# Kernel tuning notes

Measured on AMD Instinct MI355X. Metric: run time of the kernel, lower is better.

## Reference

```python
import math
import jax, jax.numpy as jnp
import numpy as np

B, N, D_MODEL, H = 2, 4096, 2048, 16
HEAD_DIM = D_MODEL // H
CHUNK = 128  # chunk length for the lightning-attention recurrence


def _slopes(n_heads):
    # ALiBi-style slopes used by lightning attention (n_heads is a power of 2)
    start = 2.0 ** (-(2.0 ** -(math.log2(n_heads) - 3)))
    return np.array([start ** (i + 1) for i in range(n_heads)], dtype=np.float32)


def setup_inputs() -> dict:
    key = jax.random.key(0)
    kx, k1, k2, k3, k4 = jax.random.split(key, 5)
    scale = 1.0 / math.sqrt(D_MODEL)
    x = jax.random.normal(kx, (B, N, D_MODEL), dtype=jnp.float32)
    w_qkv = jax.random.normal(k1, (3 * D_MODEL, D_MODEL), dtype=jnp.float32) * scale
    b_qkv = jax.random.normal(k2, (3 * D_MODEL,), dtype=jnp.float32) * 0.01
    w_out = jax.random.normal(k3, (D_MODEL, D_MODEL), dtype=jnp.float32) * scale
    b_out = jax.random.normal(k4, (D_MODEL,), dtype=jnp.float32) * 0.01
    return {"x": x, "w_qkv": w_qkv, "b_qkv": b_qkv, "w_out": w_out, "b_out": b_out}


def _lightning_attn(q, k, v):
    # q,k,v: (B, H, N, d). Causal linear attention with per-head decay lam:
    #   S_t = lam * S_{t-1} + k_t v_t^T ;  o_t = q_t S_t
    b, h, n, d = q.shape
    nc = n // CHUNK
    lam = jnp.exp(-jnp.asarray(_slopes(h)))  # (H,)

    pos = jnp.arange(CHUNK, dtype=jnp.float32)
    decay_q = lam[:, None] ** (pos + 1.0)            # (H, C) inter-chunk q scaling
    decay_k = lam[:, None] ** (CHUNK - 1.0 - pos)    # (H, C) state-update k scaling
    diff = pos[:, None] - pos[None, :]
    causal = diff >= 0
    dmask = jnp.where(causal, lam[:, None, None] ** jnp.maximum(diff, 0.0), 0.0)  # (H,C,C)
    lam_c = lam ** CHUNK                              # (H,)

    def to_chunks(t):
        return t.reshape(b, h, nc, CHUNK, d).transpose(2, 0, 1, 3, 4)  # (nc,B,H,C,d)

    qc, kc, vc = to_chunks(q), to_chunks(k), to_chunks(v)

    def step(S, inp):
        qb, kb, vb = inp  # each (B,H,C,d); S: (B,H,d,d)
        inter = jnp.einsum('bhcd,bhde->bhce', qb * decay_q[None, :, :, None], S)
        scores = jnp.einsum('bhcd,bhed->bhce', qb, kb) * dmask[None]
        intra = jnp.einsum('bhce,bhed->bhcd', scores, vb)
        S_new = lam_c[None, :, None, None] * S + jnp.einsum(
            'bhcd,bhce->bhde', kb * decay_k[None, :, :, None], vb)
        return S_new, inter + intra

    S0 = jnp.zeros((b, h, d, d), dtype=q.dtype)
    _, out = jax.lax.scan(step, S0, (qc, kc, vc))  # out: (nc,B,H,C,d)
    return out.transpose(1, 2, 0, 3, 4).reshape(b, h, n, d)


def reference(x, w_qkv, b_qkv, w_out, b_out):
    b, n, dm = x.shape
    qkv = x @ w_qkv.T + b_qkv                         # (B,N,3D)
    q, k, v = jnp.split(qkv, 3, axis=-1)
    def heads(t):
        return t.reshape(b, n, H, HEAD_DIM).transpose(0, 2, 1, 3)  # (B,H,N,d)
    attn = _lightning_attn(heads(q), heads(k), heads(v))
    attn = attn.transpose(0, 2, 1, 3).reshape(b, n, dm)
    return attn @ w_out.T + b_out
```

## Files before the change

kernel.cpp:

```cpp
#include <hip/hip_runtime.h>
#include <stdint.h>

#define DM    2048
#define NSEQ  4096
#define BB    2
#define NH    16
#define HD    128
#define CHK   128
#define NCHK  32
#define NBH   (BB*NH)
#define MTOT  (BB*NSEQ)
#define N3    (3*DM)

typedef unsigned short u16;
typedef unsigned int   u32;
typedef __attribute__((ext_vector_type(8))) short s16x8;
typedef __attribute__((ext_vector_type(4))) short s16x4;
typedef __attribute__((ext_vector_type(4))) float f32x4;
typedef __attribute__((ext_vector_type(2))) unsigned short u16x2;

__device__ __forceinline__ float b2f(u16 b){ u32 u = ((u32)b) << 16; float f; __builtin_memcpy(&f,&u,4); return f; }
__device__ __forceinline__ u16 f2b(float f){ u32 u; __builtin_memcpy(&u,&f,4); u += 0x7fffu + ((u>>16)&1u); return (u16)(u>>16); }

__device__ __forceinline__ void gload16(const u16* g, u16* l){
  __builtin_amdgcn_global_load_lds((const __attribute__((address_space(1))) void*)g,
                                   (__attribute__((address_space(3))) void*)l, 16, 0, 0);
}

__global__ __launch_bounds__(256) void conv_bf16(const float* __restrict__ src,
                                                 u16* __restrict__ dst, int n4)
{
  for (int i = blockIdx.x*blockDim.x + threadIdx.x; i < n4; i += gridDim.x*blockDim.x){
    f32x4 v = *(const f32x4*)(src + (size_t)i*4);
    s16x4 o;
    #pragma unroll
    for (int j=0;j<4;j++) o[j] = (short)f2b(v[j]);
    *(s16x4*)(dst + (size_t)i*4) = o;
  }
}


#define GEMM256_CORE(GA_, GB_)                                                  \
  const int tid  = threadIdx.x;                                                 \
  const int lane = tid & 63;                                                    \
  const int w    = tid >> 6;                                                    \
  const int wm_i = w >> 2, wn_i = w & 3;                                        \
  const int m0 = blockIdx.y << 8;                                               \
  const int n0 = blockIdx.x << 8;                                               \
                  \
  const int q_  = (lane*16) ^ (((lane>>5)&1) << 5);                             \
  const int sgr = q_ >> 6;                                                      \
  const int sgc = (q_ & 63) >> 1;                                               \
  const u16* gA = GA_ + (size_t)(m0 + w*32 + sgr)*DM + sgc;                     \
  const u16* gB = GB_ + (size_t)(n0 + w*32 + sgr)*DM + sgc;                     \
  const int l15 = lane & 15, lg = lane >> 4;                                    \
  const int swz = ((lg*16) ^ (((l15>>3)&1) << 5)) >> 1;          \
  const int arow = (wm_i*128 + l15)*32 + swz;                                   \
  const int brow = (wn_i*64  + l15)*32 + swz;                                   \
  f32x4 acc[8][4];                                                              \
  _Pragma("unroll")                                                             \
  for (int m=0;m<8;m++)                                                         \
    _Pragma("unroll")                                                           \
    for (int n=0;n<4;n++) acc[m][n] = f32x4{0.f,0.f,0.f,0.f};                   \
  s16x8 bfr[4];                                                                 \
  auto STAGE_A = [&](int set, int kt){                                          \
    const u16* a = gA + kt*32;                                                  \
    u16* la = lds + set + w*1024;                                               \
    gload16(a,         la);                                                     \
    gload16(a + 16*DM, la + 512);                                               \
  };                                                                            \
  auto STAGE_B = [&](int set, int kt){                                          \
    const u16* b = gB + kt*32;                                                  \
    u16* la = lds + set + w*1024;                                               \
    gload16(b,         la + 8192);                                              \
    gload16(b + 16*DM, la + 8704);                                              \
  };                                                                            \
  auto COMPA = [&](int set){                                                    \
    const u16* base = lds + set;                                                \
    s16x8 af[4];                                                                \
    _Pragma("unroll")                                                           \
    for (int n=0;n<4;n++) bfr[n] = *(const s16x8*)(base + 8192 + brow + n*512); \
    _Pragma("unroll")                                                           \
    for (int m=0;m<4;m++) af[m] = *(const s16x8*)(base + arow + m*512);         \
    __builtin_amdgcn_s_setprio(1);                                              \
    _Pragma("unroll")                                                           \
    for (int m=0;m<4;m++)                                                       \
      _Pragma("unroll")                                                         \
      for (int n=0;n<4;n++)                                                     \
        acc[m][n] = __builtin_amdgcn_mfma_f32_16x16x32_bf16(af[m], bfr[n], acc[m][n], 0,0,0); \
    __builtin_amdgcn_s_setprio(0);                                              \
  };                                                                            \
  auto COMPB = [&](int set){                                                    \
    const u16* base = lds + set;                                                \
    s16x8 af[4];                                                                \
    _Pragma("unroll")                                                           \
    for (int m=0;m<4;m++) af[m] = *(const s16x8*)(base + arow + (m+4)*512);     \
    __builtin_amdgcn_s_setprio(1);                                              \
    _Pragma("unroll")                                                           \
    for (int m=0;m<4;m++)                                                       \
      _Pragma("unroll")                                                         \
      for (int n=0;n<4;n++)                                                     \
        acc[m+4][n] = __builtin_amdgcn_mfma_f32_16x16x32_bf16(af[m], bfr[n], acc[m+4][n], 0,0,0); \
    __builtin_amdgcn_s_setprio(0);                                              \
  };                                                                            \
  STAGE_A(0, 0);     STAGE_B(0, 0);                                             \
  STAGE_A(16384, 1); STAGE_B(16384, 1);                                         \
  STAGE_A(32768, 2); STAGE_B(32768, 2);                                         \
  asm volatile("s_waitcnt vmcnt(8)" ::: "memory");                              \
  __builtin_amdgcn_s_barrier();                                                 \
  int s0=0, s1=16384, s2=32768, s3=49152;                                       \
  for (int t=0; t<64; ++t){                                                     \
    if (t < 61) STAGE_A(s3, t+3);                                               \
    COMPA(s0);                                                                  \
    __builtin_amdgcn_s_barrier();                                               \
    if (t < 61) STAGE_B(s3, t+3);                                               \
    COMPB(s0);                                                                  \
    if      (t < 61)  { asm volatile("s_waitcnt vmcnt(8)" ::: "memory"); }      \
    else if (t == 61) { asm volatile("s_waitcnt vmcnt(4)" ::: "memory"); }      \
    else if (t == 62) { asm volatile("s_waitcnt vmcnt(0)" ::: "memory"); }      \
    __builtin_amdgcn_s_barrier();                                               \
    const int tmp=s0; s0=s1; s1=s2; s2=s3; s3=tmp;                              \
  }

__global__ __launch_bounds__(512, 2) void gemm_qkv(const u16* __restrict__ Xb,
    const u16* __restrict__ Wb, const float* __restrict__ bias,
    u16* __restrict__ Qb, u16* __restrict__ Kb, u16* __restrict__ Vb)
{
  __shared__ u16 lds[4*16384];
  GEMM256_CORE(Xb, Wb)

  #pragma unroll
  for (int n=0;n<4;n++){
    const int gn = n0 + wn_i*64 + n*16 + l15;
    const float bv = bias[gn];
    const int which = gn >> 11;
    const int h = (gn >> 7) & 15;
    const int e = gn & 127;
    u16* base_ = (which==0) ? Qb : ((which==1) ? Kb : Vb);
    #pragma unroll
    for (int m=0;m<8;m++){
      #pragma unroll
      for (int r=0;r<4;r++){
        const int gm = m0 + wm_i*128 + m*16 + lg*4 + r;
        const int b  = gm >> 12;
        const int tt = gm & (NSEQ-1);
        base_[(((size_t)(b*NH + h))*NSEQ + tt)*HD + e] = f2b(acc[m][n][r] + bv);
      }
    }
  }
}

__global__ __launch_bounds__(512, 2) void gemm_out(const u16* __restrict__ Ab,
    const u16* __restrict__ Wb, const float* __restrict__ bias,
    float* __restrict__ Out)
{
  __shared__ u16 lds[4*16384];
  GEMM256_CORE(Ab, Wb)

  #pragma unroll
  for (int n=0;n<4;n++){
    const int gn = n0 + wn_i*64 + n*16 + l15;
    const float bv = bias[gn];
    #pragma unroll
    for (int m=0;m<8;m++){
      #pragma unroll
      for (int r=0;r<4;r++){
        const int gm = m0 + wm_i*128 + m*16 + lg*4 + r;
        Out[(size_t)gm*DM + gn] = acc[m][n][r] + bv;
      }
    }
  }
}

__global__ __launch_bounds__(256) void chunk_kv(const u16* __restrict__ Kb,
    const u16* __restrict__ Vb, u16* __restrict__ USb)
{
  __shared__ short Kt[128][152];
  __shared__ short Vt[128][152];
  const int tid = threadIdx.x;
  const int blk = blockIdx.x;
  const int c  = blk & (NCHK-1);
  const int bh = blk >> 5;
  const int h  = bh & (NH-1);
  const float slope = exp2f(-0.5f*(float)(h+1));

  const u16* kg = Kb + ((size_t)bh*NSEQ + (size_t)c*CHK)*HD;
  const u16* vg = Vb + ((size_t)bh*NSEQ + (size_t)c*CHK)*HD;

  const int e0 = (tid & 63) * 2;
  const int tq = tid >> 6;
  #pragma unroll
  for (int it=0; it<4; it++){
    const int tb = it*32 + tq*8;
    s16x8 k0v, k1v, v0v, v1v;
    #pragma unroll
    for (int j=0;j<8;j++){
      const int t = tb + j;
      u16x2 kv = *(const u16x2*)(kg + (size_t)t*HD + e0);
      u16x2 vv = *(const u16x2*)(vg + (size_t)t*HD + e0);
      const float dk = expf(-slope*(float)(CHK-1-t));
      k0v[j] = (short)f2b(b2f(kv[0])*dk);
      k1v[j] = (short)f2b(b2f(kv[1])*dk);
      v0v[j] = (short)vv[0];
      v1v[j] = (short)vv[1];
    }
    *(s16x8*)&Kt[e0  ][tb] = k0v;
    *(s16x8*)&Kt[e0+1][tb] = k1v;
    *(s16x8*)&Vt[e0  ][tb] = v0v;
    *(s16x8*)&Vt[e0+1][tb] = v1v;
  }
  __syncthreads();

  const int lane = tid & 63;
  const int l15 = lane & 15, lg = lane >> 4;
  const int w = tid >> 6;
  const int wm = (w >> 1) << 6, wn = (w & 1) << 6;
  f32x4 acc[4][4];
  #pragma unroll
  for (int i=0;i<4;i++)
    #pragma unroll
    for (int j=0;j<4;j++) acc[i][j] = f32x4{0.f,0.f,0.f,0.f};

  #pragma unroll
  for (int ks=0; ks<4; ks++){
    const int kk = ks*32 + lg*8;
    s16x8 af[4], bf[4];
    #pragma unroll
    for (int m=0;m<4;m++) af[m] = *(const s16x8*)&Kt[wm + m*16 + l15][kk];
    #pragma unroll
    for (int n=0;n<4;n++) bf[n] = *(const s16x8*)&Vt[wn + n*16 + l15][kk];
    #pragma unroll
    for (int m=0;m<4;m++)
      #pragma unroll
      for (int n=0;n<4;n++)
        acc[m][n] = __builtin_amdgcn_mfma_f32_16x16x32_bf16(af[m], bf[n], acc[m][n], 0,0,0);
  }

  u16* up = USb + (size_t)blk*(HD*HD);
  #pragma unroll
  for (int m=0;m<4;m++)
    #pragma unroll
    for (int n=0;n<4;n++)
      #pragma unroll
      for (int r=0;r<4;r++){
        const int d = wm + m*16 + lg*4 + r;
        const int f = wn + n*16 + l15;
        up[d*HD + f] = f2b(acc[m][n][r]);
      }
}

__global__ __launch_bounds__(256) void scan_state(u16* __restrict__ USb)
{
  const int bh = blockIdx.x >> 3;
  const int rs = blockIdx.x & 7;
  const int tid = threadIdx.x;
  const int h = bh & (NH-1);
  const float slope = exp2f(-0.5f*(float)(h+1));
  const float lamC = expf(-slope*(float)CHK);
  float s[8];
  #pragma unroll
  for (int i=0;i<8;i++) s[i]=0.f;
  u16* base = USb + (size_t)bh*NCHK*HD*HD + rs*2048;
  const int off = tid*8;
  for (int c=0;c<NCHK;c++){
    u16* p = base + (size_t)c*HD*HD + off;
    s16x8 u = *(const s16x8*)p;
    s16x8 wv;
    #pragma unroll
    for (int j=0;j<8;j++) wv[j] = (short)f2b(s[j]);
    *(s16x8*)p = wv;
    #pragma unroll
    for (int j=0;j<8;j++) s[j] = lamC*s[j] + b2f((u16)u[j]);
  }
}

__global__ __launch_bounds__(512) void attn_chunk(
    const u16* __restrict__ Qb, const u16* __restrict__ Kb, const u16* __restrict__ Vb,
    const u16* __restrict__ Sb, u16* __restrict__ ATT)
{
  __shared__ short lds[73728];
  short* Qs = lds;
  short* Ks = lds + 17408;
  short* Vt = lds + 34816;
  short* St = lds + 54272;

  const int tid = threadIdx.x;
  const int blk = blockIdx.x;
  const int c  = blk & (NCHK-1);
  const int bh = blk >> 5;
  const int b  = bh >> 4, h = bh & 15;
  const float slope = exp2f(-0.5f*(float)(h+1));

  const size_t qoff = ((size_t)bh*NSEQ + (size_t)c*CHK)*HD;

  #pragma unroll
  for (int i=0;i<4;i++){
    const int lin = i*4096 + tid*8;
    const int r = lin >> 7, e = lin & 127;
    *(s16x8*)&Qs[r*136 + e] = *(const s16x8*)(Qb + qoff + lin);
    *(s16x8*)&Ks[r*136 + e] = *(const s16x8*)(Kb + qoff + lin);
  }
  {
    const int f0 = (tid & 63)*2;
    const int tq = tid >> 6;
    const u16* vg = Vb + qoff;
    const u16* sg = Sb + ((size_t)bh*NCHK + c)*HD*HD;
    #pragma unroll
    for (int it=0; it<2; it++){
      const int t0 = it*64 + tq*8;
      s16x8 v0v, v1v, s0v, s1v;
      #pragma unroll
      for (int j=0;j<8;j++){
        u16x2 v2 = *(const u16x2*)(vg + (size_t)(t0+j)*HD + f0);
        u16x2 s2 = *(const u16x2*)(sg + (size_t)(t0+j)*HD + f0);
        v0v[j]=(short)v2[0]; v1v[j]=(short)v2[1];
        s0v[j]=(short)s2[0]; s1v[j]=(short)s2[1];
      }
      *(s16x8*)&Vt[(f0  )*152 + t0] = v0v;
      *(s16x8*)&Vt[(f0+1)*152 + t0] = v1v;
      *(s16x8*)&St[(f0  )*152 + t0] = s0v;
      *(s16x8*)&St[(f0+1)*152 + t0] = s1v;
    }
  }
  __syncthreads();

  const int lane = tid & 63;
  const int l15 = lane & 15, lg = lane >> 4;
  const int w = tid >> 6;
  const int wrow = (w >> 1) << 5;
  const int wcol = (w & 1) << 6;

  f32x4 accs[2][4], acco[2][4];
  #pragma unroll
  for (int m=0;m<2;m++)
    #pragma unroll
    for (int n=0;n<4;n++){ accs[m][n]=f32x4{0.f,0.f,0.f,0.f}; acco[m][n]=f32x4{0.f,0.f,0.f,0.f}; }

  #pragma unroll
  for (int ks=0; ks<4; ks++){
    const int kk = ks*32 + lg*8;
    s16x8 qa[2], kb_[4], sb_[4];
    #pragma unroll
    for (int m=0;m<2;m++) qa[m] = *(const s16x8*)&Qs[(wrow + m*16 + l15)*136 + kk];
    #pragma unroll
    for (int n=0;n<4;n++){
      kb_[n] = *(const s16x8*)&Ks[(wcol + n*16 + l15)*136 + kk];
      sb_[n] = *(const s16x8*)&St[(wcol + n*16 + l15)*152 + kk];
    }
    #pragma unroll
    for (int m=0;m<2;m++)
      #pragma unroll
      for (int n=0;n<4;n++){
        accs[m][n] = __builtin_amdgcn_mfma_f32_16x16x32_bf16(qa[m], kb_[n], accs[m][n], 0,0,0);
        acco[m][n] = __builtin_amdgcn_mfma_f32_16x16x32_bf16(qa[m], sb_[n], acco[m][n], 0,0,0);
      }
  }
  __syncthreads();

  #pragma unroll
  for (int m=0;m<2;m++){
    #pragma unroll
    for (int r=0;r<4;r++){
      const int t = wrow + m*16 + lg*4 + r;
      const float dq = expf(-slope*(float)(t+1));
      #pragma unroll
      for (int n=0;n<4;n++){
        const int s = wcol + n*16 + l15;
        float v = accs[m][n][r];
        v = (t >= s) ? v*expf(-slope*(float)(t-s)) : 0.f;
        Ks[t*136 + s] = (short)f2b(v);
        acco[m][n][r] *= dq;
      }
    }
  }
  __syncthreads();

  #pragma unroll
  for (int ks=0; ks<4; ks++){
    const int kk = ks*32 + lg*8;
    s16x8 sa[2], vb_[4];
    #pragma unroll
    for (int m=0;m<2;m++) sa[m] = *(const s16x8*)&Ks[(wrow + m*16 + l15)*136 + kk];
    #pragma unroll
    for (int n=0;n<4;n++) vb_[n] = *(const s16x8*)&Vt[(wcol + n*16 + l15)*152 + kk];
    #pragma unroll
    for (int m=0;m<2;m++)
      #pragma unroll
      for (int n=0;n<4;n++)
        acco[m][n] = __builtin_amdgcn_mfma_f32_16x16x32_bf16(sa[m], vb_[n], acco[m][n], 0,0,0);
  }

  u16* op = ATT + ((size_t)(b*NSEQ + c*CHK))*DM + h*HD;
  #pragma unroll
  for (int m=0;m<2;m++)
    #pragma unroll
    for (int n=0;n<4;n++)
      #pragma unroll
      for (int r=0;r<4;r++){
        const int t = wrow + m*16 + lg*4 + r;
        const int f = wcol + n*16 + l15;
        op[(size_t)t*DM + f] = f2b(acco[m][n][r]);
      }
}

extern "C" void kernel_launch(void* const* d_in, const int* in_sizes, int n_in,
                              void* d_out, int out_size, void* d_ws, size_t ws_size,
                              hipStream_t stream)
{
  const float* x     = (const float*)d_in[0];
  const float* w_qkv = (const float*)d_in[1];
  const float* b_qkv = (const float*)d_in[2];
  const float* w_out = (const float*)d_in[3];
  const float* b_out = (const float*)d_in[4];
  float* out = (float*)d_out;

  char* ws = (char*)d_ws;
  const size_t SZ = (size_t)MTOT * DM * sizeof(u16);
  u16* Qb    = (u16*)(ws);
  u16* Kb    = (u16*)(ws + SZ);
  u16* Vb    = (u16*)(ws + 2*SZ);
  u16* USb   = (u16*)(ws + 3*SZ);
  u16* ATT   = (u16*)(ws + 4*SZ);
  u16* Xb    = ATT;
  u16* Wqkvb = USb;
  u16* Woutb = Kb;

  conv_bf16 <<<dim3(2048), 256, 0, stream>>>(x,     Xb,    MTOT*DM/4);
  conv_bf16 <<<dim3(2048), 256, 0, stream>>>(w_qkv, Wqkvb, N3*DM/4);
  gemm_qkv  <<<dim3(N3/256,  MTOT/256), 512, 0, stream>>>(Xb, Wqkvb, b_qkv, Qb, Kb, Vb);
  chunk_kv  <<<dim3(NBH*NCHK),          256, 0, stream>>>(Kb, Vb, USb);
  scan_state<<<dim3(NBH*8),             256, 0, stream>>>(USb);
  attn_chunk<<<dim3(NBH*NCHK),          512, 0, stream>>>(Qb, Kb, Vb, USb, ATT);
  conv_bf16 <<<dim3(1024), 256, 0, stream>>>(w_out, Woutb, DM*DM/4);
  gemm_out  <<<dim3(DM/256,  MTOT/256), 512, 0, stream>>>(ATT, Woutb, b_out, out);
}
```

Baseline: 403.2 us.

## Restructure GEMM main loop into explicit ping-pong phases and remap blocks per XCD

Splits each k-step of the 256x256 GEMM core into explicit phases. LDS fragment loads and global prefetch issue first, then a barrier, then an MFMA cluster, with sched_barriers keeping the compiler from interleaving them. This follows a ping-pong style where the two waves per SIMD alternate between memory and compute. It also remaps the linear workgroup index so consecutive tiles land on the same XCD, which should improve L2 reuse. The extra barriers per iteration add sync cost and could serialize work if the two resident workgroups don't alternate as intended.

```diff
diff --git a/kernel.cpp b/kernel.cpp
--- a/kernel.cpp
+++ b/kernel.cpp
@@ -45,8 +45,13 @@
   const int lane = tid & 63;                                                    \
   const int w    = tid >> 6;                                                    \
   const int wm_i = w >> 2, wn_i = w & 3;                                        \
-  const int m0 = blockIdx.y << 8;                                               \
-  const int n0 = blockIdx.x << 8;                                               \
+  int bx = blockIdx.x, by = blockIdx.y;                                         \
+  { const int gx = gridDim.x; const int nwg = gx*gridDim.y;                     \
+    const int cpx = nwg >> 3; const int lin = by*gx + bx;                       \
+    const int t_ = (lin & 7)*cpx + (lin >> 3);                                  \
+    bx = t_ % gx; by = t_ / gx; }                                               \
+  const int m0 = by << 8;                                                       \
+  const int n0 = bx << 8;                                                       \
                   \
   const int q_  = (lane*16) ^ (((lane>>5)&1) << 5);                             \
   const int sgr = q_ >> 6;                                                      \
@@ -62,7 +67,6 @@
   for (int m=0;m<8;m++)                                                         \
     _Pragma("unroll")                                                           \
     for (int n=0;n<4;n++) acc[m][n] = f32x4{0.f,0.f,0.f,0.f};                   \
-  s16x8 bfr[4];                                                                 \
   auto STAGE_A = [&](int set, int kt){                                          \
     const u16* a = gA + kt*32;                                                  \
     u16* la = lds + set + w*1024;                                               \
@@ -75,34 +79,6 @@
     gload16(b,         la + 8192);                                              \
     gload16(b + 16*DM, la + 8704);                                              \
   };                                                                            \
-  auto COMPA = [&](int set){                                                    \
-    const u16* base = lds + set;                                                \
-    s16x8 af[4];                                                                \
-    _Pragma("unroll")                                                           \
-    for (int n=0;n<4;n++) bfr[n] = *(const s16x8*)(base + 8192 + brow + n*512); \
-    _Pragma("unroll")                                                           \
-    for (int m=0;m<4;m++) af[m] = *(const s16x8*)(base + arow + m*512);         \
-    __builtin_amdgcn_s_setprio(1);                                              \
-    _Pragma("unroll")                                                           \
-    for (int m=0;m<4;m++)                                                       \
-      _Pragma("unroll")                                                         \
-      for (int n=0;n<4;n++)                                                     \
-        acc[m][n] = __builtin_amdgcn_mfma_f32_16x16x32_bf16(af[m], bfr[n], acc[m][n], 0,0,0); \
-    __builtin_amdgcn_s_setprio(0);                                              \
-  };                                                                            \
-  auto COMPB = [&](int set){                                                    \
-    const u16* base = lds + set;                                                \
-    s16x8 af[4];                                                                \
-    _Pragma("unroll")                                                           \
-    for (int m=0;m<4;m++) af[m] = *(const s16x8*)(base + arow + (m+4)*512);     \
-    __builtin_amdgcn_s_setprio(1);                                              \
-    _Pragma("unroll")                                                           \
-    for (int m=0;m<4;m++)                                                       \
-      _Pragma("unroll")                                                         \
-      for (int n=0;n<4;n++)                                                     \
-        acc[m+4][n] = __builtin_amdgcn_mfma_f32_16x16x32_bf16(af[m], bfr[n], acc[m+4][n], 0,0,0); \
-    __builtin_amdgcn_s_setprio(0);                                              \
-  };                                                                            \
   STAGE_A(0, 0);     STAGE_B(0, 0);                                             \
   STAGE_A(16384, 1); STAGE_B(16384, 1);                                         \
   STAGE_A(32768, 2); STAGE_B(32768, 2);                                         \
@@ -110,14 +86,46 @@
   __builtin_amdgcn_s_barrier();                                                 \
   int s0=0, s1=16384, s2=32768, s3=49152;                                       \
   for (int t=0; t<64; ++t){                                                     \
+    const u16* base = lds + s0;                                                 \
+         \
+    s16x8 af0[4], af1[4], bfr[4];                                               \
+    _Pragma("unroll")                                                           \
+    for (int n=0;n<4;n++) bfr[n] = *(const s16x8*)(base + 8192 + brow + n*512); \
+    _Pragma("unroll")                                                           \
+    for (int m=0;m<4;m++) af0[m] = *(const s16x8*)(base + arow + m*512);        \
     if (t < 61) STAGE_A(s3, t+3);                                               \
-    COMPA(s0);                                                                  \
+    __builtin_amdgcn_sched_barrier(0);                                          \
     __builtin_amdgcn_s_barrier();                                               \
+    asm volatile("s_waitcnt lgkmcnt(0)" ::: "memory");                          \
+    __builtin_amdgcn_sched_barrier(0);                                          \
+    __builtin_amdgcn_s_setprio(1);                                              \
+    _Pragma("unroll")                                                           \
+    for (int m=0;m<4;m++)                                                       \
+      _Pragma("unroll")                                                         \
+      for (int n=0;n<4;n++)                                                     \
+        acc[m][n] = __builtin_amdgcn_mfma_f32_16x16x32_bf16(af0[m], bfr[n], acc[m][n], 0,0,0); \
+    __builtin_amdgcn_s_setprio(0);                                              \
+    __builtin_amdgcn_sched_barrier(0);                                          \
+    __builtin_amdgcn_s_barrier();                                               \
+      \
+    _Pragma("unroll")                                                           \
+    for (int m=0;m<4;m++) af1[m] = *(const s16x8*)(base + arow + (m+4)*512);    \
     if (t < 61) STAGE_B(s3, t+3);                                               \
-    COMPB(s0);                                                                  \
     if      (t < 61)  { asm volatile("s_waitcnt vmcnt(8)" ::: "memory"); }      \
     else if (t == 61) { asm volatile("s_waitcnt vmcnt(4)" ::: "memory"); }      \
     else if (t == 62) { asm volatile("s_waitcnt vmcnt(0)" ::: "memory"); }      \
+    __builtin_amdgcn_sched_barrier(0);                                          \
+    __builtin_amdgcn_s_barrier();                                               \
+    asm volatile("s_waitcnt lgkmcnt(0)" ::: "memory");                          \
+    __builtin_amdgcn_sched_barrier(0);                                          \
+    __builtin_amdgcn_s_setprio(1);                                              \
+    _Pragma("unroll")                                                           \
+    for (int m=0;m<4;m++)                                                       \
+      _Pragma("unroll")                                                         \
+      for (int n=0;n<4;n++)                                                     \
+        acc[m+4][n] = __builtin_amdgcn_mfma_f32_16x16x32_bf16(af1[m], bfr[n], acc[m+4][n], 0,0,0); \
+    __builtin_amdgcn_s_setprio(0);                                              \
+    __builtin_amdgcn_sched_barrier(0);                                          \
     __builtin_amdgcn_s_barrier();                                               \
     const int tmp=s0; s0=s1; s1=s2; s2=s3; s3=tmp;                              \
   }
```

New measurement: 397.5 us. Within noise of the previous version (-1.4%).
